# Kernel optimization log

Hardware: AMD Instinct MI355X
Metric: run time of the kernel (lower is better)

## Reference

```python
import jax, jax.numpy as jnp
import numpy as np

B, N, D, V, Y = 4, 4096, 512, 50257, 16000

def setup_inputs() -> dict:
    key = jax.random.key(0)
    ks = jax.random.split(key, 5)
    # token ids in [1, V): avoid pad_id=0 so no attention row is fully -inf
    M_s = jax.random.randint(ks[0], (B, N), 1, V)
    E_v = jax.random.normal(ks[1], (V, D), jnp.float32) * 0.02
    E_y = jax.random.normal(ks[2], (Y, D), jnp.float32) * 0.02
    s = 1.0 / np.sqrt(D)  # kaiming_uniform(a=sqrt(5)) bound for [D,D]
    W_A = jax.random.uniform(ks[3], (D, D), jnp.float32, minval=-s, maxval=s)
    W_O = jax.random.uniform(ks[4], (D, D), jnp.float32, minval=-s, maxval=s)
    gamma = jnp.ones((D,), jnp.float32)
    beta = jnp.zeros((D,), jnp.float32)
    return {"M_s": M_s, "E_v": E_v, "E_y": E_y, "W_A": W_A, "W_O": W_O,
            "gamma": gamma, "beta": beta}

def _layer_norm(x, g, b, eps=1e-5):
    mu = jnp.mean(x, axis=-1, keepdims=True)
    var = jnp.mean(jnp.square(x - mu), axis=-1, keepdims=True)
    return (x - mu) * jax.lax.rsqrt(var + eps) * g + b

def reference(M_s, E_v, E_y, W_A, W_O, gamma, beta):
    # Self-attention branch (v_q=None), dropout in eval mode (identity).
    X = E_v[M_s]                                   # [B, N, D]
    mask = (M_s != 0)                              # [B, N] padding mask
    # logits = (X @ W_A) @ X^T
    logits = jnp.einsum('bnd,de,bme->bnm', X, W_A, X)   # [B, N, N]
    logits = jnp.where(mask[:, None, :], logits, -jnp.inf)
    # positional + causal bias: D = -|i-j| with future (i<j) set to -inf
    i = jnp.arange(N, dtype=jnp.float32)[:, None]
    j = jnp.arange(N, dtype=jnp.float32)[None, :]
    dist = i - j
    bias = jnp.where(dist >= 0, -dist, -jnp.inf)        # [N, N]
    A = jax.nn.softmax(logits + bias, axis=-1)          # [B, N, N]
    Q_c = jnp.einsum('bnm,bmd,de->bne', A, X, W_O)      # [B, N, D]
    H = _layer_norm(Q_c + X, gamma, beta)               # [B, N, D]
    y_logits = jnp.einsum('bnd,yd->bny', H, E_y)        # [B, N, Y]
    return y_logits, A
```

## Files before the change

### kernel.cpp

```cpp
#include <hip/hip_runtime.h>


#define DEVINL __device__ __forceinline__

typedef __attribute__((ext_vector_type(8))) short bf16x8;
typedef __attribute__((ext_vector_type(4))) float f32x4;
typedef unsigned short u16;

#define BB 4
#define NN 4096
#define DD 512
#define YY 16000
#define YPAD 16128
#define ROWS (BB * NN)

DEVINL u16 f2bf(float x) {
  unsigned u = __float_as_uint(x);
  return (u16)((u + 0x7fffu + ((u >> 16) & 1u)) >> 16);
}

DEVINL float bf2f(u16 h) { return __uint_as_float((unsigned)h << 16); }

DEVINL void gload16(const void* g, void* l) {
  __builtin_amdgcn_global_load_lds(
      (const __attribute__((address_space(1))) void*)g,
      (__attribute__((address_space(3))) void*)l, 16, 0, 0);
}

DEVINL void zero_acc(f32x4 acc[4][4]) {
#pragma unroll
  for (int m = 0; m < 4; ++m)
#pragma unroll
    for (int n = 0; n < 4; ++n) {
      acc[m][n][0] = 0.f; acc[m][n][1] = 0.f;
      acc[m][n][2] = 0.f; acc[m][n][3] = 0.f;
    }
}

DEVINL void gemm_bt_core(const u16* __restrict__ A, int lda,
                         const u16* __restrict__ Bm, int ldb, int ksteps,
                         u16* sA, u16* sB, f32x4 acc[4][4], int tid) {
  const int lane = tid & 63, w = tid >> 6;
  const int wr = (w >> 1) * 64, wc = (w & 1) * 64;
  const int c0 = w * 128 + lane, c1 = c0 + 64;
  const u16* gA0 = A + (size_t)(c0 >> 2) * lda + (c0 & 3) * 8;
  const u16* gA1 = A + (size_t)(c1 >> 2) * lda + (c1 & 3) * 8;
  const u16* gB0 = Bm + (size_t)(c0 >> 2) * ldb + (c0 & 3) * 8;
  const u16* gB1 = Bm + (size_t)(c1 >> 2) * ldb + (c1 & 3) * 8;
  u16* lA0 = sA + w * 1024;  u16* lA1 = lA0 + 512;
  u16* lB0 = sB + w * 1024;  u16* lB1 = lB0 + 512;
  const int fr = lane & 15, fk = (lane >> 4) * 8;

  for (int kt = 0; kt < ksteps; ++kt) {
    __syncthreads();
    gload16(gA0 + kt * 32, lA0);
    gload16(gA1 + kt * 32, lA1);
    gload16(gB0 + kt * 32, lB0);
    gload16(gB1 + kt * 32, lB1);
    __syncthreads();
    bf16x8 af[4], bfv[4];
#pragma unroll
    for (int m = 0; m < 4; ++m)
      af[m] = *(const bf16x8*)(sA + (wr + m * 16 + fr) * 32 + fk);
#pragma unroll
    for (int n = 0; n < 4; ++n)
      bfv[n] = *(const bf16x8*)(sB + (wc + n * 16 + fr) * 32 + fk);
#pragma unroll
    for (int m = 0; m < 4; ++m)
#pragma unroll
      for (int n = 0; n < 4; ++n)
        acc[m][n] = __builtin_amdgcn_mfma_f32_16x16x32_bf16(af[m], bfv[n],
                                                            acc[m][n], 0, 0, 0);
  }
}

#define C256_STAGE(kt, buf)                                    \
  {                                                            \
    const u16* a0 = Ag + (kt) * 64;                            \
    const u16* b0 = Bg + (kt) * 64;                            \
    u16* Lb = lds + (buf) * 32768;                             \
    gload16(a0 + offE0, Lb + d0);                              \
    gload16(a0 + offE1, Lb + d1);                              \
    gload16(a0 + 65536 + offE0, Lb + 8192 + d0);               \
    gload16(a0 + 65536 + offE1, Lb + 8192 + d1);               \
    gload16(b0 + offE0, Lb + 16384 + d0);                      \
    gload16(b0 + offE1, Lb + 16384 + d1);                      \
    gload16(b0 + 65536 + offE0, Lb + 24576 + d0);              \
    gload16(b0 + 65536 + offE1, Lb + 24576 + d1);              \
  }

DEVINL void core256(const u16* __restrict__ Ag, const u16* __restrict__ Bg,
                    u16* lds, f32x4 (&acc)[8][4], int tid) {
  const int lane = tid & 63, w = tid >> 6;
  const int wm = w >> 2, wn = w & 3;

  int offE0, offE1;
  {
    int q = tid;
    int r = (((q >> 6) >> 1) << 4) | ((q >> 2) & 15);
    int c = (((q >> 6) & 1) << 5) |
            (((q & 3) << 3) ^ (((q >> 5) & 1) << 4) ^ (((q >> 4) & 1) << 3));
    offE0 = r * DD + c;
    q = 512 + tid;
    r = (((q >> 6) >> 1) << 4) | ((q >> 2) & 15);
    c = (((q >> 6) & 1) << 5) |
        (((q & 3) << 3) ^ (((q >> 5) & 1) << 4) ^ (((q >> 4) & 1) << 3));
    offE1 = r * DD + c;
  }
  const int d0 = w * 512, d1 = 4096 + w * 512;

  int x = (lane & 15) * 64 + ((lane >> 4) & 3) * 16;
  int fxu = (x ^ (((x >> 9) & 1) << 5) ^ (((x >> 8) & 1) << 4)) >> 1;

#pragma unroll
  for (int m = 0; m < 8; ++m)
#pragma unroll
    for (int n = 0; n < 4; ++n) {
      acc[m][n][0] = 0.f; acc[m][n][1] = 0.f;
      acc[m][n][2] = 0.f; acc[m][n][3] = 0.f;
    }

  C256_STAGE(0, 0);
  C256_STAGE(1, 1);
  asm volatile("s_waitcnt vmcnt(8)" ::: "memory");
  __syncthreads();

  for (int c = 0; c < 8; ++c) {
    const u16* L = lds + (c & 1) * 32768;
    const u16* pa = L + wm * 8192;
    const u16* pb = L + 16384 + (wn >> 1) * 8192 + (wn & 1) * 4096;
    bf16x8 af[4][2], bf[4][2];
#pragma unroll
    for (int n = 0; n < 2; ++n)
#pragma unroll
      for (int ks = 0; ks < 2; ++ks)
        bf[n][ks] = *(const bf16x8*)(pb + (n * 2 + ks) * 512 + fxu);
#pragma unroll
    for (int m = 0; m < 4; ++m)
#pragma unroll
      for (int ks = 0; ks < 2; ++ks)
        af[m][ks] = *(const bf16x8*)(pa + (m * 2 + ks) * 512 + fxu);
    __builtin_amdgcn_s_setprio(1);
#pragma unroll
    for (int m = 0; m < 4; ++m)
#pragma unroll
      for (int n = 0; n < 2; ++n)
#pragma unroll
        for (int ks = 0; ks < 2; ++ks)
          acc[m][n] = __builtin_amdgcn_mfma_f32_16x16x32_bf16(
              af[m][ks], bf[n][ks], acc[m][n], 0, 0, 0);
    __builtin_amdgcn_s_setprio(0);
#pragma unroll
    for (int n = 2; n < 4; ++n)
#pragma unroll
      for (int ks = 0; ks < 2; ++ks)
        bf[n][ks] = *(const bf16x8*)(pb + (n * 2 + ks) * 512 + fxu);
    __builtin_amdgcn_s_setprio(1);
#pragma unroll
    for (int m = 0; m < 4; ++m)
#pragma unroll
      for (int n = 2; n < 4; ++n)
#pragma unroll
        for (int ks = 0; ks < 2; ++ks)
          acc[m][n] = __builtin_amdgcn_mfma_f32_16x16x32_bf16(
              af[m][ks], bf[n][ks], acc[m][n], 0, 0, 0);
    __builtin_amdgcn_s_setprio(0);
#pragma unroll
    for (int m = 0; m < 4; ++m)
#pragma unroll
      for (int ks = 0; ks < 2; ++ks)
        af[m][ks] = *(const bf16x8*)(pa + ((m + 4) * 2 + ks) * 512 + fxu);
    __builtin_amdgcn_s_setprio(1);
#pragma unroll
    for (int m = 0; m < 4; ++m)
#pragma unroll
      for (int n = 0; n < 2; ++n)
#pragma unroll
        for (int ks = 0; ks < 2; ++ks)
          acc[m + 4][n] = __builtin_amdgcn_mfma_f32_16x16x32_bf16(
              af[m][ks], bf[n][ks], acc[m + 4][n], 0, 0, 0);
#pragma unroll
    for (int m = 0; m < 4; ++m)
#pragma unroll
      for (int n = 2; n < 4; ++n)
#pragma unroll
        for (int ks = 0; ks < 2; ++ks)
          acc[m + 4][n] = __builtin_amdgcn_mfma_f32_16x16x32_bf16(
              af[m][ks], bf[n][ks], acc[m + 4][n], 0, 0, 0);
    __builtin_amdgcn_s_setprio(0);

    __syncthreads();
    if (c < 6) {
      C256_STAGE(c + 2, c & 1);
      asm volatile("s_waitcnt vmcnt(8)" ::: "memory");
    } else if (c == 6) {
      asm volatile("s_waitcnt vmcnt(0)" ::: "memory");
    }
    __syncthreads();
  }
}

__global__ __launch_bounds__(256) void prep_all(const int* __restrict__ Ms,
                                                const float* __restrict__ Ev,
                                                const float* __restrict__ WA,
                                                const float* __restrict__ WO,
                                                const float* __restrict__ Ey,
                                                u16* __restrict__ Xb,
                                                u16* __restrict__ WAt,
                                                u16* __restrict__ WOt,
                                                u16* __restrict__ Eyb) {
  __shared__ u16 t[64][65];
  int bx = blockIdx.x, tid = threadIdx.x;
  if (bx < 8192) {
    int row = bx * 2 + (tid >> 7);
    int t4 = tid & 127;
    int tok = Ms[row];
    float4 v = *(const float4*)(Ev + (size_t)tok * DD + t4 * 4);
    *(ushort4*)(Xb + (size_t)row * DD + t4 * 4) =
        make_ushort4(f2bf(v.x), f2bf(v.y), f2bf(v.z), f2bf(v.w));
  } else if (bx < 8320) {
    int k = bx - 8192;
    const float* W = (k < 64) ? WA : WO;
    u16* Wt = (k < 64) ? WAt : WOt;
    k &= 63;
    int dt = k >> 3, et = k & 7;
#pragma unroll
    for (int p = 0; p < 16; ++p) {
      int e = tid + 256 * p; int r = e >> 6, c = e & 63;
      t[r][c] = f2bf(W[(size_t)(dt * 64 + r) * DD + et * 64 + c]);
    }
    __syncthreads();
#pragma unroll
    for (int p = 0; p < 16; ++p) {
      int e = tid + 256 * p; int r = e >> 6, c = e & 63;
      Wt[(size_t)(et * 64 + r) * DD + dt * 64 + c] = t[c][r];
    }
  } else {
    size_t i4 = (size_t)(bx - 8320) * 256 + tid;
    size_t row = i4 >> 7;
    ushort4 h;
    if (row < YY) {
      float4 v = *(const float4*)(Ey + i4 * 4);
      h = make_ushort4(f2bf(v.x), f2bf(v.y), f2bf(v.z), f2bf(v.w));
    } else {
      h = make_ushort4(0, 0, 0, 0);
    }
    *(ushort4*)(Eyb + i4 * 4) = h;
  }
}

__global__ __launch_bounds__(256) void k2_xw(const u16* __restrict__ Xb,
                                             const u16* __restrict__ WAt,
                                             u16* __restrict__ XWb) {
  __shared__ u16 sA[4096], sB[4096];
  f32x4 acc[4][4]; zero_acc(acc);
  int tid = threadIdx.x;
  size_t row0 = (size_t)blockIdx.x * 128, col0 = (size_t)blockIdx.y * 128;
  gemm_bt_core(Xb + row0 * DD, DD, WAt + col0 * DD, DD, DD / 32, sA, sB, acc, tid);
  int lane = tid & 63, w = tid >> 6;
  int wr = (w >> 1) * 64, wc = (w & 1) * 64;
  int cr = (lane >> 4) * 4, cc = lane & 15;
#pragma unroll
  for (int m = 0; m < 4; ++m)
#pragma unroll
    for (int n = 0; n < 4; ++n)
#pragma unroll
      for (int r = 0; r < 4; ++r) {
        size_t gi = row0 + wr + m * 16 + cr + r;
        size_t gj = col0 + wc + n * 16 + cc;
        XWb[gi * DD + gj] = f2bf(acc[m][n][r]);
      }
}

__global__ __launch_bounds__(256) void k_wot(const u16* __restrict__ WOt,
                                             const u16* __restrict__ Xb,
                                             u16* __restrict__ XWoT) {
  __shared__ u16 sA[4096], sB[4096];
  f32x4 acc[4][4]; zero_acc(acc);
  int tid = threadIdx.x;
  int et = blockIdx.x, it = blockIdx.y, b = blockIdx.z;
  const u16* Ap = WOt + (size_t)et * 128 * DD;
  const u16* Bp = Xb + ((size_t)b * NN + it * 128) * DD;
  gemm_bt_core(Ap, DD, Bp, DD, DD / 32, sA, sB, acc, tid);
  int lane = tid & 63, w = tid >> 6;
  int wr = (w >> 1) * 64, wc = (w & 1) * 64;
  int cr = (lane >> 4) * 4, cc = lane & 15;
#pragma unroll
  for (int m = 0; m < 4; ++m)
#pragma unroll
    for (int n = 0; n < 4; ++n)
#pragma unroll
      for (int r = 0; r < 4; ++r) {
        size_t e = (size_t)et * 128 + wr + m * 16 + cr + r;
        size_t i = (size_t)it * 128 + wc + n * 16 + cc;
        XWoT[((size_t)b * DD + e) * NN + i] = f2bf(acc[m][n][r]);
      }
}

__global__ __launch_bounds__(256) void k3_scores(const u16* __restrict__ XWb,
                                                 const u16* __restrict__ Xb,
                                                 u16* __restrict__ Ebf) {
  int t = blockIdx.x, b = blockIdx.z;
  int ib = (int)((sqrtf(8.f * (float)t + 1.f) - 1.f) * 0.5f);
  while ((ib + 1) * (ib + 2) / 2 <= t) ++ib;
  while (ib * (ib + 1) / 2 > t) --ib;
  int jb = t - ib * (ib + 1) / 2;
  __shared__ u16 sA[4096], sB[4096];
  f32x4 acc[4][4]; zero_acc(acc);
  int tid = threadIdx.x;
  const u16* Ap = XWb + ((size_t)b * NN + ib * 128) * DD;
  const u16* Bp = Xb  + ((size_t)b * NN + jb * 128) * DD;
  gemm_bt_core(Ap, DD, Bp, DD, DD / 32, sA, sB, acc, tid);
  int lane = tid & 63, w = tid >> 6;
  int wr = (w >> 1) * 64, wc = (w & 1) * 64;
  int cr = (lane >> 4) * 4, cc = lane & 15;
  u16* Eb = Ebf + (size_t)b * NN * NN;
#pragma unroll
  for (int m = 0; m < 4; ++m)
#pragma unroll
    for (int n = 0; n < 4; ++n)
#pragma unroll
      for (int r = 0; r < 4; ++r) {
        int i = ib * 128 + wr + m * 16 + cr + r;
        int j = jb * 128 + wc + n * 16 + cc;
        float e = (j > i) ? 0.f : __expf(acc[m][n][r] - (float)(i - j));
        Eb[(size_t)i * NN + j] = f2bf(e);
      }
}

__global__ __launch_bounds__(256) void k5_ax(const u16* __restrict__ Ebf,
                                             const u16* __restrict__ XWoT,
                                             u16* __restrict__ Qcb) {
  int u = blockIdx.x;
  int half = u >> 8, v = u & 255;
  int ib = v & 31; if (half) ib = 31 - ib;
  int db = (v >> 5) & 3;
  int b = (half << 1) | (v >> 7);
  __shared__ u16 sA[4096], sB[4096];
  f32x4 acc[4][4]; zero_acc(acc);
  int tid = threadIdx.x;
  const u16* Ap = Ebf + ((size_t)b * NN + ib * 128) * NN;
  const u16* Bp = XWoT + ((size_t)b * DD + db * 128) * NN;
  gemm_bt_core(Ap, NN, Bp, NN, (ib + 1) * 4, sA, sB, acc, tid);
  int lane = tid & 63, w = tid >> 6;
  int wr = (w >> 1) * 64, wc = (w & 1) * 64;
  int cr = (lane >> 4) * 4, cc = lane & 15;
#pragma unroll
  for (int m = 0; m < 4; ++m)
#pragma unroll
    for (int n = 0; n < 4; ++n)
#pragma unroll
      for (int r = 0; r < 4; ++r) {
        int i = ib * 128 + wr + m * 16 + cr + r;
        int d = db * 128 + wc + n * 16 + cc;
        Qcb[((size_t)b * NN + i) * DD + d] = f2bf(acc[m][n][r]);
      }
}

__global__ __launch_bounds__(256) void k4_softmax(const u16* __restrict__ Ebf,
                                                  float* __restrict__ Aout,
                                                  float* __restrict__ invb) {
  __shared__ u16 srow[NN];
  __shared__ float red[4];
  size_t row = blockIdx.x;
  int i = (int)(row & (NN - 1));
  const u16* E = Ebf + row * (size_t)NN;
  float* S = Aout + row * (size_t)NN;
  int len = i + 1, tid = threadIdx.x;
  int padend = (len + 127) & ~127;
  int nc = padend >> 3;
  for (int v = tid; v < nc; v += 256)
    *(uint4*)(srow + v * 8) = *(const uint4*)(E + v * 8);
  __syncthreads();
  float l = 0.f;
  for (int v = tid; v < nc; v += 256) {
    uint4 x = *(const uint4*)(srow + v * 8);
    l += bf2f((u16)(x.x & 0xffff)) + bf2f((u16)(x.x >> 16));
    l += bf2f((u16)(x.y & 0xffff)) + bf2f((u16)(x.y >> 16));
    l += bf2f((u16)(x.z & 0xffff)) + bf2f((u16)(x.z >> 16));
    l += bf2f((u16)(x.w & 0xffff)) + bf2f((u16)(x.w >> 16));
  }
#pragma unroll
  for (int o = 32; o; o >>= 1) l += __shfl_xor(l, o);
  if ((tid & 63) == 0) red[tid >> 6] = l;
  __syncthreads();
  float inv = 1.f / (red[0] + red[1] + red[2] + red[3]);
  if (tid == 0) invb[row] = inv;
  for (int v = tid; v < NN / 4; v += 256) {
    int k = v * 4;
    float4 a = make_float4(0.f, 0.f, 0.f, 0.f);
    if (k < padend) {
      ushort4 e = *(const ushort4*)(srow + k);
      a = make_float4(bf2f(e.x) * inv, bf2f(e.y) * inv,
                      bf2f(e.z) * inv, bf2f(e.w) * inv);
    }
    *(float4*)(S + k) = a;
  }
}

__global__ __launch_bounds__(128) void k6b_ln(const u16* __restrict__ Qcb,
                                              const u16* __restrict__ Xb,
                                              const float* __restrict__ invb,
                                              const float* __restrict__ gamma,
                                              const float* __restrict__ beta,
                                              u16* __restrict__ Hb) {
  int row = blockIdx.x, tid = threadIdx.x;
  float inv = invb[row];
  ushort4 qu = *(const ushort4*)(Qcb + (size_t)row * DD + tid * 4);
  ushort4 xu = *(const ushort4*)(Xb + (size_t)row * DD + tid * 4);
  float v0 = bf2f(qu.x) * inv + bf2f(xu.x), v1 = bf2f(qu.y) * inv + bf2f(xu.y);
  float v2 = bf2f(qu.z) * inv + bf2f(xu.z), v3 = bf2f(qu.w) * inv + bf2f(xu.w);
  float s = v0 + v1 + v2 + v3;
  float s2 = v0 * v0 + v1 * v1 + v2 * v2 + v3 * v3;
#pragma unroll
  for (int o = 32; o; o >>= 1) { s += __shfl_xor(s, o); s2 += __shfl_xor(s2, o); }
  __shared__ float r1[2], r2[2];
  int lane = tid & 63, w = tid >> 6;
  if (lane == 0) { r1[w] = s; r2[w] = s2; }
  __syncthreads();
  s = r1[0] + r1[1]; s2 = r2[0] + r2[1];
  float mu = s * (1.f / 512.f);
  float var = s2 * (1.f / 512.f) - mu * mu;
  float rs = 1.f / sqrtf(var + 1e-5f);
  float4 g  = *(const float4*)(gamma + tid * 4);
  float4 be = *(const float4*)(beta + tid * 4);
  ushort4 h = make_ushort4(f2bf((v0 - mu) * rs * g.x + be.x),
                           f2bf((v1 - mu) * rs * g.y + be.y),
                           f2bf((v2 - mu) * rs * g.z + be.z),
                           f2bf((v3 - mu) * rs * g.w + be.w));
  *(ushort4*)(Hb + (size_t)row * DD + tid * 4) = h;
}

__global__ __launch_bounds__(512, 2) void k7_logits(const u16* __restrict__ Hb,
                                                    const u16* __restrict__ Eyb,
                                                    float* __restrict__ Yout) {
  __shared__ u16 lds[65536];
  const int tid = threadIdx.x;
  const int lane = tid & 63, w = tid >> 6;
  const int wm = w >> 2, wn = w & 3;

  int id = blockIdx.x;
  int swz = (id & 7) * (4032 / 8) + (id >> 3);
  size_t row0 = (size_t)(swz & 63) * 256;
  size_t col0 = (size_t)(swz >> 6) * 256;

  f32x4 acc[8][4];
  core256(Hb + row0 * DD, Eyb + col0 * DD, lds, acc, tid);

  const int cr = (lane >> 4) * 4, cc = lane & 15;
#pragma unroll
  for (int m = 0; m < 8; ++m)
#pragma unroll
    for (int n = 0; n < 4; ++n) {
      size_t gj = col0 + wn * 64 + n * 16 + cc;
      if (gj < YY) {
        size_t gi = row0 + wm * 128 + m * 16 + cr;
#pragma unroll
        for (int rr = 0; rr < 4; ++rr)
          Yout[(gi + rr) * (size_t)YY + gj] = acc[m][n][rr];
      }
    }
}

extern "C" void kernel_launch(void* const* d_in, const int* in_sizes, int n_in,
                              void* d_out, int out_size, void* d_ws, size_t ws_size,
                              hipStream_t stream) {
  (void)in_sizes; (void)n_in; (void)out_size; (void)ws_size;
  const int*   Ms    = (const int*)d_in[0];
  const float* Ev    = (const float*)d_in[1];
  const float* Ey    = (const float*)d_in[2];
  const float* WA    = (const float*)d_in[3];
  const float* WO    = (const float*)d_in[4];
  const float* gamma = (const float*)d_in[5];
  const float* beta  = (const float*)d_in[6];

  float* Yout = (float*)d_out;
  float* Aout = Yout + (size_t)BB * NN * YY;

  char* w = (char*)d_ws;
  u16* Xb   = (u16*)w; w += (size_t)ROWS * DD * 2;
  u16* XWoT = (u16*)w; w += (size_t)BB * DD * NN * 2;
  u16* XWb  = (u16*)w; w += (size_t)ROWS * DD * 2;
  u16* Hb   = (u16*)w; w += (size_t)ROWS * DD * 2;
  u16* WAt  = (u16*)w; w += (size_t)DD * DD * 2;
  u16* WOt  = (u16*)w; w += (size_t)DD * DD * 2;
  u16* Eyb  = (u16*)w; w += (size_t)YPAD * DD * 2;
  u16* Ebf  = (u16*)w; w += (size_t)ROWS * NN * 2;
  float* invb = (float*)w; w += (size_t)ROWS * 4;
  u16* Qcb = XWb;

  prep_all<<<16384, 256, 0, stream>>>(Ms, Ev, WA, WO, Ey, Xb, WAt, WOt, Eyb);
  k_wot<<<dim3(DD / 128, NN / 128, BB), 256, 0, stream>>>(WOt, Xb, XWoT);
  k2_xw<<<dim3(ROWS / 128, DD / 128), 256, 0, stream>>>(Xb, WAt, XWb);
  k3_scores<<<dim3(528, 1, BB), 256, 0, stream>>>(XWb, Xb, Ebf);
  k5_ax<<<512, 256, 0, stream>>>(Ebf, XWoT, Qcb);
  k4_softmax<<<ROWS, 256, 0, stream>>>(Ebf, Aout, invb);
  k6b_ln<<<ROWS, 128, 0, stream>>>(Qcb, Xb, invb, gamma, beta, Hb);
  k7_logits<<<dim3(64 * 63), 512, 0, stream>>>(Hb, Eyb, Yout);
}
```

Baseline: 808.8 us.

## Merge projection GEMMs into one launch and zero masked attention tiles in scores kernel

The two independent projection GEMMs (X·W_A and W_O·X^T) now run as one launch over 1024 blocks, which removes a launch and lets the two grids share the GPU. The scores kernel writes zeros into the strictly-upper causal tiles of the attention output, using each lower-triangle block to cover its mirrored upper tile. The softmax kernel then writes only up to the padded diagonal end of each row, not the full row. This moves the zero writes to blocks that otherwise finish early, at the cost of some extra scattered stores in the scores kernel.

```diff
diff --git a/kernel.cpp b/kernel.cpp
--- a/kernel.cpp
+++ b/kernel.cpp
@@ -249,57 +249,54 @@
   }
 }
 
-__global__ __launch_bounds__(256) void k2_xw(const u16* __restrict__ Xb,
-                                             const u16* __restrict__ WAt,
-                                             u16* __restrict__ XWb) {
+__global__ __launch_bounds__(256) void k2w(const u16* __restrict__ Xb,
+                                           const u16* __restrict__ WAt,
+                                           const u16* __restrict__ WOt,
+                                           u16* __restrict__ XWb,
+                                           u16* __restrict__ XWoT) {
   __shared__ u16 sA[4096], sB[4096];
   f32x4 acc[4][4]; zero_acc(acc);
-  int tid = threadIdx.x;
-  size_t row0 = (size_t)blockIdx.x * 128, col0 = (size_t)blockIdx.y * 128;
-  gemm_bt_core(Xb + row0 * DD, DD, WAt + col0 * DD, DD, DD / 32, sA, sB, acc, tid);
+  int tid = threadIdx.x, bx = blockIdx.x;
   int lane = tid & 63, w = tid >> 6;
   int wr = (w >> 1) * 64, wc = (w & 1) * 64;
   int cr = (lane >> 4) * 4, cc = lane & 15;
-#pragma unroll
-  for (int m = 0; m < 4; ++m)
-#pragma unroll
-    for (int n = 0; n < 4; ++n)
-#pragma unroll
-      for (int r = 0; r < 4; ++r) {
-        size_t gi = row0 + wr + m * 16 + cr + r;
-        size_t gj = col0 + wc + n * 16 + cc;
-        XWb[gi * DD + gj] = f2bf(acc[m][n][r]);
-      }
-}
-
-__global__ __launch_bounds__(256) void k_wot(const u16* __restrict__ WOt,
-                                             const u16* __restrict__ Xb,
-                                             u16* __restrict__ XWoT) {
-  __shared__ u16 sA[4096], sB[4096];
-  f32x4 acc[4][4]; zero_acc(acc);
-  int tid = threadIdx.x;
-  int et = blockIdx.x, it = blockIdx.y, b = blockIdx.z;
-  const u16* Ap = WOt + (size_t)et * 128 * DD;
-  const u16* Bp = Xb + ((size_t)b * NN + it * 128) * DD;
-  gemm_bt_core(Ap, DD, Bp, DD, DD / 32, sA, sB, acc, tid);
-  int lane = tid & 63, w = tid >> 6;
-  int wr = (w >> 1) * 64, wc = (w & 1) * 64;
-  int cr = (lane >> 4) * 4, cc = lane & 15;
-#pragma unroll
-  for (int m = 0; m < 4; ++m)
-#pragma unroll
-    for (int n = 0; n < 4; ++n)
-#pragma unroll
-      for (int r = 0; r < 4; ++r) {
-        size_t e = (size_t)et * 128 + wr + m * 16 + cr + r;
-        size_t i = (size_t)it * 128 + wc + n * 16 + cc;
-        XWoT[((size_t)b * DD + e) * NN + i] = f2bf(acc[m][n][r]);
-      }
+  if (bx < 512) {
+    size_t row0 = (size_t)(bx >> 2) * 128, col0 = (size_t)(bx & 3) * 128;
+    gemm_bt_core(Xb + row0 * DD, DD, WAt + col0 * DD, DD, DD / 32, sA, sB,
+                 acc, tid);
+#pragma unroll
+    for (int m = 0; m < 4; ++m)
+#pragma unroll
+      for (int n = 0; n < 4; ++n)
+#pragma unroll
+        for (int r = 0; r < 4; ++r) {
+          size_t gi = row0 + wr + m * 16 + cr + r;
+          size_t gj = col0 + wc + n * 16 + cc;
+          XWb[gi * DD + gj] = f2bf(acc[m][n][r]);
+        }
+  } else {
+    int j = bx - 512;
+    int et = j & 3, it = (j >> 2) & 31, b = j >> 7;
+    const u16* Ap = WOt + (size_t)et * 128 * DD;
+    const u16* Bp = Xb + ((size_t)b * NN + it * 128) * DD;
+    gemm_bt_core(Ap, DD, Bp, DD, DD / 32, sA, sB, acc, tid);
+#pragma unroll
+    for (int m = 0; m < 4; ++m)
+#pragma unroll
+      for (int n = 0; n < 4; ++n)
+#pragma unroll
+        for (int r = 0; r < 4; ++r) {
+          size_t e = (size_t)et * 128 + wr + m * 16 + cr + r;
+          size_t i = (size_t)it * 128 + wc + n * 16 + cc;
+          XWoT[((size_t)b * DD + e) * NN + i] = f2bf(acc[m][n][r]);
+        }
+  }
 }
 
 __global__ __launch_bounds__(256) void k3_scores(const u16* __restrict__ XWb,
                                                  const u16* __restrict__ Xb,
-                                                 u16* __restrict__ Ebf) {
+                                                 u16* __restrict__ Ebf,
+                                                 float* __restrict__ Aout) {
   int t = blockIdx.x, b = blockIdx.z;
   int ib = (int)((sqrtf(8.f * (float)t + 1.f) - 1.f) * 0.5f);
   while ((ib + 1) * (ib + 2) / 2 <= t) ++ib;
@@ -326,6 +323,16 @@
         float e = (j > i) ? 0.f : __expf(acc[m][n][r] - (float)(i - j));
         Eb[(size_t)i * NN + j] = f2bf(e);
       }
+  if (jb < ib) {
+    float* Az = Aout + (size_t)b * NN * NN + ((size_t)jb * 128) * NN + ib * 128;
+    f32x4 z = {0.f, 0.f, 0.f, 0.f};
+#pragma unroll
+    for (int p = 0; p < 16; ++p) {
+      int e = tid + p * 256;
+      int r = e >> 5, c4 = e & 31;
+      *(f32x4*)(Az + (size_t)r * NN + c4 * 4) = z;
+    }
+  }
 }
 
 __global__ __launch_bounds__(256) void k5_ax(const u16* __restrict__ Ebf,
@@ -386,14 +393,11 @@
   __syncthreads();
   float inv = 1.f / (red[0] + red[1] + red[2] + red[3]);
   if (tid == 0) invb[row] = inv;
-  for (int v = tid; v < NN / 4; v += 256) {
+  for (int v = tid; v < (padend >> 2); v += 256) {
     int k = v * 4;
-    float4 a = make_float4(0.f, 0.f, 0.f, 0.f);
-    if (k < padend) {
-      ushort4 e = *(const ushort4*)(srow + k);
-      a = make_float4(bf2f(e.x) * inv, bf2f(e.y) * inv,
-                      bf2f(e.z) * inv, bf2f(e.w) * inv);
-    }
+    ushort4 e = *(const ushort4*)(srow + k);
+    float4 a = make_float4(bf2f(e.x) * inv, bf2f(e.y) * inv,
+                           bf2f(e.z) * inv, bf2f(e.w) * inv);
     *(float4*)(S + k) = a;
   }
 }
@@ -490,9 +494,8 @@
   u16* Qcb = XWb;
 
   prep_all<<<16384, 256, 0, stream>>>(Ms, Ev, WA, WO, Ey, Xb, WAt, WOt, Eyb);
-  k_wot<<<dim3(DD / 128, NN / 128, BB), 256, 0, stream>>>(WOt, Xb, XWoT);
-  k2_xw<<<dim3(ROWS / 128, DD / 128), 256, 0, stream>>>(Xb, WAt, XWb);
-  k3_scores<<<dim3(528, 1, BB), 256, 0, stream>>>(XWb, Xb, Ebf);
+  k2w<<<1024, 256, 0, stream>>>(Xb, WAt, WOt, XWb, XWoT);
+  k3_scores<<<dim3(528, 1, BB), 256, 0, stream>>>(XWb, Xb, Ebf, Aout);
   k5_ax<<<512, 256, 0, stream>>>(Ebf, XWoT, Qcb);
   k4_softmax<<<ROWS, 256, 0, stream>>>(Ebf, Aout, invb);
   k6b_ln<<<ROWS, 128, 0, stream>>>(Qcb, Xb, invb, gamma, beta, Hb);
```

New measurement: 824.4 us. Within noise of the previous version (+1.9%).
